# Kernel tuning notes

Measured on AMD Instinct MI355X. Metric: run time of the kernel, lower is better.

The kernel has to match this reference:

```python
import jax, jax.numpy as jnp
import numpy as np
from jax import lax

EPS = 1e-5
K = 16  # MixedOp.self.k


def conv(x, w, stride=1, pad=0, dil=1, groups=1):
    return lax.conv_general_dilated(
        x, w, (stride, stride), [(pad, pad), (pad, pad)],
        rhs_dilation=(dil, dil), feature_group_count=groups,
        dimension_numbers=('NCHW', 'OIHW', 'NCHW'))


def bn(x):
    # BatchNorm2d(affine=False) in training mode: normalize with batch stats
    m = jnp.mean(x, axis=(0, 2, 3), keepdims=True)
    v = jnp.var(x, axis=(0, 2, 3), keepdims=True)
    return (x - m) * lax.rsqrt(v + EPS)


def maxpool3(x):
    return lax.reduce_window(x, -jnp.inf, lax.max, (1, 1, 3, 3), (1, 1, 1, 1),
                             [(0, 0), (0, 0), (1, 1), (1, 1)])


def avgpool3(x):
    # AvgPool2d(3, stride=1, padding=1, count_include_pad=False)
    s = lax.reduce_window(x, 0., lax.add, (1, 1, 3, 3), (1, 1, 1, 1),
                          [(0, 0), (0, 0), (1, 1), (1, 1)])
    c = lax.reduce_window(jnp.ones_like(x), 0., lax.add, (1, 1, 3, 3),
                          (1, 1, 1, 1), [(0, 0), (0, 0), (1, 1), (1, 1)])
    return s / c


def sep_conv(x, dw1, pw1, dw2, pw2):
    C = x.shape[1]
    p = dw1.shape[-1] // 2
    h = jax.nn.relu(x)
    h = conv(h, dw1, pad=p, groups=C)
    h = bn(conv(h, pw1))
    h = jax.nn.relu(h)
    h = conv(h, dw2, pad=p, groups=C)
    return bn(conv(h, pw2))


def dil_conv(x, dw, pw):
    C = x.shape[1]
    p = (dw.shape[-1] // 2) * 2  # dilation=2 padding (3x3->2, 5x5->4)
    h = jax.nn.relu(x)
    h = conv(h, dw, pad=p, dil=2, groups=C)
    return bn(conv(h, pw))


def setup_inputs() -> dict:
    key = jax.random.key(0)
    C, B, H, W = 256, 32, 64, 64
    c_op = C // K  # 16 channels fed to each candidate op
    ks = jax.random.split(key, 17)
    g = lambda k, shp, fan: jax.random.normal(k, shp, jnp.float32) / np.sqrt(fan)
    return {
        'x': jax.random.normal(ks[0], (B, C, H, W), jnp.float32),
        # ChannelAttention se: 1x1 convs, reduction=2
        'ca_w1': g(ks[1], (C // 2, C, 1, 1), C),
        'ca_w2': g(ks[2], (C, C // 2, 1, 1), C // 2),
        # sep_conv_3x3 (two dw+pw stages)
        's3_dw1': g(ks[3], (c_op, 1, 3, 3), 9),
        's3_pw1': g(ks[4], (c_op, c_op, 1, 1), c_op),
        's3_dw2': g(ks[5], (c_op, 1, 3, 3), 9),
        's3_pw2': g(ks[6], (c_op, c_op, 1, 1), c_op),
        # sep_conv_5x5
        's5_dw1': g(ks[7], (c_op, 1, 5, 5), 25),
        's5_pw1': g(ks[8], (c_op, c_op, 1, 1), c_op),
        's5_dw2': g(ks[9], (c_op, 1, 5, 5), 25),
        's5_pw2': g(ks[10], (c_op, c_op, 1, 1), c_op),
        # dil_conv_3x3 / dil_conv_5x5
        'd3_dw': g(ks[11], (c_op, 1, 3, 3), 9),
        'd3_pw': g(ks[12], (c_op, c_op, 1, 1), c_op),
        'd5_dw': g(ks[13], (c_op, 1, 5, 5), 25),
        'd5_pw': g(ks[14], (c_op, c_op, 1, 1), c_op),
        # AttentionModule fc: channel = 8*c_op = 128, ratio = 8
        'at_w1': g(ks[15], (c_op, 8 * c_op), 8 * c_op),  # Linear(128->16)
        'at_w2': g(ks[16], (8 * c_op, c_op), c_op),      # Linear(16->128)
    }


def reference(x, ca_w1, ca_w2, s3_dw1, s3_pw1, s3_dw2, s3_pw2,
              s5_dw1, s5_pw1, s5_dw2, s5_pw2, d3_dw, d3_pw, d5_dw, d5_pw,
              at_w1, at_w2):
    B, C, H, W = x.shape
    c_sel = C // K  # number of selected channels (16)

    # ---- ChannelAttention ----
    mx = jnp.max(x, axis=(2, 3), keepdims=True)   # [B,C,1,1]
    av = jnp.mean(x, axis=(2, 3), keepdims=True)
    se = lambda z: conv(jax.nn.relu(conv(z, ca_w1)), ca_w2)
    num_list = jax.nn.sigmoid(se(mx) + se(av))    # [B,C,1,1]

    aux = x                                       # auxiliary_op = Identity (stride=1)
    xg = x * num_list

    # ---- top-k channel routing ----
    slist = jnp.sum(num_list, axis=0).reshape(C)  # sum over batch
    _, idx = lax.top_k(slist, c_sel)              # sorted, largest first
    xt = xg[:, idx]                               # gather [B,c_sel,H,W]

    # ---- 8 candidate branches (DARTS PRIMITIVES, stride=1) ----
    branches = [
        jnp.zeros_like(xt),                       # none
        bn(maxpool3(xt)),                         # max_pool_3x3 + BN
        bn(avgpool3(xt)),                         # avg_pool_3x3 + BN
        xt,                                       # skip_connect (Identity)
        sep_conv(xt, s3_dw1, s3_pw1, s3_dw2, s3_pw2),
        sep_conv(xt, s5_dw1, s5_pw1, s5_dw2, s5_pw2),
        dil_conv(xt, d3_dw, d3_pw),
        dil_conv(xt, d5_dw, d5_pw),
    ]
    temp = jnp.concatenate(branches, axis=1)      # [B, 8*c_sel, H, W]

    # ---- AttentionModule ----
    y = jnp.mean(temp, axis=(2, 3))               # [B, 8*c_sel]
    y = jax.nn.sigmoid(jax.nn.relu(y @ at_w1.T) @ at_w2.T)
    att = temp * y[:, :, None, None]
    op_attention = jnp.sum(y.reshape(B, 8, c_sel), axis=(0, 2))  # [8]

    # sum the 8 branch chunks
    out = jnp.sum(att.reshape(B, 8, c_sel, H, W), axis=1)

    # scatter back into gated x, then residual add
    xg = xg.at[:, idx].set(out)
    return xg + aux, op_attention
```

## Files before the change

kernel.cpp:

```cpp
#include <hip/hip_runtime.h>
#include <math.h>

static constexpr int B = 32, C = 256, HW = 4096, CS = 16;
static constexpr int BHW = B * HW;
static constexpr size_t IMG = (size_t)B * CS * HW;

static constexpr size_t OFF_S     = 0;
static constexpr size_t OFF_SQ    = 4096;
static constexpr size_t OFF_U     = 8192;
static constexpr size_t ACC_FLOATS= 8256;
static constexpr size_t OFF_MX    = 8256;
static constexpr size_t OFF_AV    = OFF_MX + 8192;
static constexpr size_t OFF_NUM   = OFF_AV + 8192;
static constexpr size_t OFF_Y     = OFF_NUM + 8192;
static constexpr size_t OFF_ACO   = OFF_Y + 4096;
static constexpr size_t OFF_BIAS  = OFF_ACO + 4096;
static constexpr size_t OFF_INT   = OFF_BIAS + 512;
static constexpr size_t OFF_R     = 42112;

__device__ inline float wave_sum(float v) {
  v += __shfl_down(v, 32); v += __shfl_down(v, 16); v += __shfl_down(v, 8);
  v += __shfl_down(v, 4);  v += __shfl_down(v, 2);  v += __shfl_down(v, 1);
  return v;
}
__device__ inline float wave_max(float v) {
  v = fmaxf(v, __shfl_down(v, 32)); v = fmaxf(v, __shfl_down(v, 16));
  v = fmaxf(v, __shfl_down(v, 8));  v = fmaxf(v, __shfl_down(v, 4));
  v = fmaxf(v, __shfl_down(v, 2));  v = fmaxf(v, __shfl_down(v, 1));
  return v;
}

__global__ __launch_bounds__(256) void k_stats(const float4* __restrict__ x,
                                               float* __restrict__ mx, float* __restrict__ av) {
  int bc = blockIdx.x;
  const float4* p = x + (size_t)bc * 1024;
  float mmax = -INFINITY, msum = 0.f;
  for (int i = threadIdx.x; i < 1024; i += 256) {
    float4 v = p[i];
    mmax = fmaxf(mmax, fmaxf(fmaxf(v.x, v.y), fmaxf(v.z, v.w)));
    msum += v.x + v.y + v.z + v.w;
  }
  __shared__ float rs[4], rm[4];
  float s = wave_sum(msum), m = wave_max(mmax);
  int w = threadIdx.x >> 6;
  if ((threadIdx.x & 63) == 0) { rs[w] = s; rm[w] = m; }
  __syncthreads();
  if (threadIdx.x == 0) {
    mx[bc] = fmaxf(fmaxf(rm[0], rm[1]), fmaxf(rm[2], rm[3]));
    av[bc] = (rs[0] + rs[1] + rs[2] + rs[3]) * (1.f / 4096.f);
  }
}

__global__ __launch_bounds__(128) void k_se(const float* __restrict__ mx, const float* __restrict__ av,
                                            const float* __restrict__ w1, const float* __restrict__ w2,
                                            float* __restrict__ num) {
  int b = blockIdx.x, t = threadIdx.x;
  __shared__ float zs[2][256], h[2][128];
  for (int i = t; i < 256; i += 128) { zs[0][i] = mx[b * 256 + i]; zs[1][i] = av[b * 256 + i]; }
  __syncthreads();
  {
    const float* wr = w1 + (size_t)t * 256;
    float am = 0.f, aa = 0.f;
    for (int i = 0; i < 256; i++) { float w = wr[i]; am = fmaf(w, zs[0][i], am); aa = fmaf(w, zs[1][i], aa); }
    h[0][t] = fmaxf(am, 0.f); h[1][t] = fmaxf(aa, 0.f);
  }
  __syncthreads();
  for (int c = t; c < 256; c += 128) {
    const float* wr = w2 + (size_t)c * 128;
    float sm = 0.f, sa = 0.f;
    for (int j = 0; j < 128; j++) { float w = wr[j]; sm = fmaf(w, h[0][j], sm); sa = fmaf(w, h[1][j], sa); }
    float s = sm + sa;
    num[b * 256 + c] = 1.f / (1.f + expf(-s));
  }
}

__global__ __launch_bounds__(256) void k_select(const float* __restrict__ num,
                                                int* __restrict__ idx, int* __restrict__ selmap,
                                                float* __restrict__ accbase) {
  __shared__ float s[256];
  int t = threadIdx.x;
  for (int i = t; i < (int)ACC_FLOATS; i += 256) accbase[i] = 0.f;
  float acc = 0.f;
  for (int b = 0; b < B; b++) acc += num[b * 256 + t];
  s[t] = acc; selmap[t] = -1;
  __syncthreads();
  float v = s[t];
  int rank = 0;
  for (int c = 0; c < 256; c++) {
    float o = s[c];
    rank += (o > v) || (o == v && c < t);
  }
  if (rank < 16) { idx[rank] = t; selmap[t] = rank; }
}

template<int KK, int DIL, int BN>
__device__ __forceinline__ void dw_full(const float* __restrict__ src, float sc,
                                        const float* __restrict__ w, float* __restrict__ dst,
                                        float* lt, float mu, float rs) {
  constexpr int P = (KK / 2) * DIL, TW = 64 + 2 * P;
  float wr[KK * KK];
#pragma unroll
  for (int i = 0; i < KK * KK; i++) wr[i] = w[i];
  for (int i = threadIdx.x; i < TW * TW; i += 256) {
    int ty = i / TW, tx = i - ty * TW;
    int y = ty - P, xx = tx - P;
    float v = 0.f;
    if ((unsigned)y < 64u && (unsigned)xx < 64u) {
      v = src[y * 64 + xx] * sc;
      if (BN) v = (v - mu) * rs;
      v = fmaxf(v, 0.f);
    }
    lt[i] = v;
  }
  __syncthreads();
  for (int i = threadIdx.x; i < HW; i += 256) {
    int y = i >> 6, xx = i & 63;
    const float* t0 = lt + y * TW + xx;
    float acc = 0.f;
#pragma unroll
    for (int a = 0; a < KK; a++)
#pragma unroll
      for (int q = 0; q < KK; q++)
        acc = fmaf(wr[a * KK + q], t0[a * DIL * TW + q * DIL], acc);
    dst[i] = acc;
  }
}

__device__ __forceinline__ void pools_full(const float* __restrict__ src, float sc,
                                           float* __restrict__ dmax, float* __restrict__ davg,
                                           float* __restrict__ S, float* __restrict__ SQ,
                                           int bk, float* lt, float* red) {
  for (int i = threadIdx.x; i < HW; i += 256) lt[i] = src[i] * sc;
  __syncthreads();
  float s1 = 0.f, q1 = 0.f, s2 = 0.f, q2 = 0.f, s3 = 0.f;
  for (int i = threadIdx.x; i < HW; i += 256) {
    int y = i >> 6, xx = i & 63;
    int y0 = max(y - 1, 0), y1 = min(y + 1, 63), x0 = max(xx - 1, 0), x1 = min(xx + 1, 63);
    float mx = -INFINITY, sm = 0.f;
    for (int yy = y0; yy <= y1; yy++)
      for (int cx = x0; cx <= x1; cx++) { float v = lt[yy * 64 + cx]; mx = fmaxf(mx, v); sm += v; }
    float av = sm / (float)((y1 - y0 + 1) * (x1 - x0 + 1));
    dmax[i] = mx; davg[i] = av;
    s1 += mx; q1 += mx * mx; s2 += av; q2 += av * av; s3 += lt[i];
  }
  s1 = wave_sum(s1); q1 = wave_sum(q1); s2 = wave_sum(s2); q2 = wave_sum(q2); s3 = wave_sum(s3);
  int w = threadIdx.x >> 6;
  if ((threadIdx.x & 63) == 0) { red[w] = s1; red[4 + w] = q1; red[8 + w] = s2; red[12 + w] = q2; red[16 + w] = s3; }
  __syncthreads();
  if (threadIdx.x == 0) {
    S[512 + bk]  = red[0] + red[1] + red[2] + red[3];
    SQ[512 + bk] = red[4] + red[5] + red[6] + red[7];
    S[1024 + bk] = red[8] + red[9] + red[10] + red[11];
    SQ[1024 + bk]= red[12] + red[13] + red[14] + red[15];
    S[1536 + bk] = red[16] + red[17] + red[18] + red[19];
  }
}

__global__ __launch_bounds__(256) void k_branchA(
    const float* __restrict__ x, const float* __restrict__ num, const int* __restrict__ idx,
    const float* __restrict__ d3dw, const float* __restrict__ d5dw,
    const float* __restrict__ s3dw1, const float* __restrict__ s5dw1,
    float* __restrict__ R, float* __restrict__ scr,
    float* __restrict__ S, float* __restrict__ SQ) {
  __shared__ float lt[72 * 72];
  __shared__ float red[20];
  int blk = blockIdx.x;
  int op = blk / 512, bk = blk - op * 512;
  int b = bk >> 4, k = bk & 15;
  int c = idx[k];
  float sc = num[b * 256 + c];
  const float* src = x + ((size_t)b * 256 + c) * HW;
  size_t o = (size_t)bk * HW;
  switch (op) {
    case 0: pools_full(src, sc, R + o, R + IMG + o, S, SQ, bk, lt, red); break;
    case 1: dw_full<3, 2, 0>(src, sc, d3dw + k * 9,  scr + 0 * IMG + o, lt, 0.f, 0.f); break;
    case 2: dw_full<5, 2, 0>(src, sc, d5dw + k * 25, scr + 1 * IMG + o, lt, 0.f, 0.f); break;
    case 3: dw_full<3, 1, 0>(src, sc, s3dw1 + k * 9,  scr + 2 * IMG + o, lt, 0.f, 0.f); break;
    case 4: dw_full<5, 1, 0>(src, sc, s5dw1 + k * 25, scr + 3 * IMG + o, lt, 0.f, 0.f); break;
  }
}

__device__ __forceinline__ void pw_tile(const float* __restrict__ in, const float* __restrict__ w16,
                                        float* __restrict__ out, float* __restrict__ sacc,
                                        float* __restrict__ qacc, int perB, int b, int tile,
                                        float* wsh, float* redS, float* redQ) {
  int t = threadIdx.x;
  wsh[t] = w16[t];
  size_t base = (size_t)b * 16 * HW + tile * 256;
  float sv[16];
#pragma unroll
  for (int i = 0; i < 16; i++) sv[i] = in[base + (size_t)i * HW + t];
  __syncthreads();
  int wv = t >> 6, lane = t & 63;
#pragma unroll
  for (int cc = 0; cc < 16; cc++) {
    float acc = 0.f;
#pragma unroll
    for (int i = 0; i < 16; i++) acc = fmaf(wsh[cc * 16 + i], sv[i], acc);
    out[base + (size_t)cc * HW + t] = acc;
    float s = wave_sum(acc), q = wave_sum(acc * acc);
    if (lane == 0) { redS[cc * 4 + wv] = s; redQ[cc * 4 + wv] = q; }
  }
  __syncthreads();
  if (t < 16) {
    float s = redS[t * 4] + redS[t * 4 + 1] + redS[t * 4 + 2] + redS[t * 4 + 3];
    float q = redQ[t * 4] + redQ[t * 4 + 1] + redQ[t * 4 + 2] + redQ[t * 4 + 3];
    int sl = perB ? b * 16 + t : t;
    atomicAdd(&sacc[sl], s); atomicAdd(&qacc[sl], q);
  }
}

__global__ __launch_bounds__(256) void k_branchB(
    const float* __restrict__ scr,
    const float* __restrict__ d3pw, const float* __restrict__ d5pw,
    const float* __restrict__ s3pw1, const float* __restrict__ s5pw1,
    float* __restrict__ R, float* __restrict__ t3, float* __restrict__ t5,
    float* __restrict__ S, float* __restrict__ SQ, float* __restrict__ U) {
  __shared__ float wsh[256], redS[64], redQ[64];
  int blk = blockIdx.x;
  int op = blk >> 9, rem = blk & 511;
  int b = rem >> 4, tile = rem & 15;
  switch (op) {
    case 0: pw_tile(scr + 0 * IMG, d3pw,  R + 4 * IMG, S + 6 * 512, SQ + 6 * 512, 1, b, tile, wsh, redS, redQ); break;
    case 1: pw_tile(scr + 1 * IMG, d5pw,  R + 5 * IMG, S + 7 * 512, SQ + 7 * 512, 1, b, tile, wsh, redS, redQ); break;
    case 2: pw_tile(scr + 2 * IMG, s3pw1, t3, U + 0,  U + 16, 0, b, tile, wsh, redS, redQ); break;
    case 3: pw_tile(scr + 3 * IMG, s5pw1, t5, U + 32, U + 48, 0, b, tile, wsh, redS, redQ); break;
  }
}

__global__ __launch_bounds__(256) void k_branchC(
    const float* __restrict__ t3, const float* __restrict__ t5,
    const float* __restrict__ s3dw2, const float* __restrict__ s5dw2,
    float* __restrict__ scr, const float* __restrict__ U) {
  __shared__ float lt[68 * 68];
  int blk = blockIdx.x;
  int op = blk >> 9, bk = blk & 511, k = bk & 15;
  size_t o = (size_t)bk * HW;
  if (op == 0) {
    float mu = U[k] * (1.f / (float)BHW);
    float var = U[16 + k] * (1.f / (float)BHW) - mu * mu;
    float rs = rsqrtf(var + 1e-5f);
    dw_full<3, 1, 1>(t3 + o, 1.f, s3dw2 + k * 9, scr + 0 * IMG + o, lt, mu, rs);
  } else {
    float mu = U[32 + k] * (1.f / (float)BHW);
    float var = U[48 + k] * (1.f / (float)BHW) - mu * mu;
    float rs = rsqrtf(var + 1e-5f);
    dw_full<5, 1, 1>(t5 + o, 1.f, s5dw2 + k * 25, scr + 1 * IMG + o, lt, mu, rs);
  }
}

__global__ __launch_bounds__(256) void k_branchD(
    const float* __restrict__ scr,
    const float* __restrict__ s3pw2, const float* __restrict__ s5pw2,
    float* __restrict__ R, float* __restrict__ S, float* __restrict__ SQ) {
  __shared__ float wsh[256], redS[64], redQ[64];
  int blk = blockIdx.x;
  int op = blk >> 9, rem = blk & 511;
  int b = rem >> 4, tile = rem & 15;
  if (op == 0) pw_tile(scr + 0 * IMG, s3pw2, R + 2 * IMG, S + 4 * 512, SQ + 4 * 512, 1, b, tile, wsh, redS, redQ);
  else         pw_tile(scr + 1 * IMG, s5pw2, R + 3 * IMG, S + 5 * 512, SQ + 5 * 512, 1, b, tile, wsh, redS, redQ);
}

__global__ __launch_bounds__(128) void k_att(const float* __restrict__ S, const float* __restrict__ SQ,
                                             const float* __restrict__ w1, const float* __restrict__ w2,
                                             float* __restrict__ y, float* __restrict__ aco,
                                             float* __restrict__ bia) {
  int b = blockIdx.x, t = threadIdx.x;
  __shared__ float ym[128], h[16], msh[8][16], rssh[8][16], ysh[128];
  int op = t >> 4, k = t & 15;
  bool isbn = (op == 1 || op == 2 || op >= 4);
  float m = 0.f, rsc = 0.f;
  {
    float ss = 0.f, qq = 0.f;
    for (int bb = 0; bb < B; bb++) { ss += S[op * 512 + bb * 16 + k]; qq += SQ[op * 512 + bb * 16 + k]; }
    if (isbn) {
      m = ss * (1.f / (float)BHW);
      float var = qq * (1.f / (float)BHW) - m * m;
      rsc = rsqrtf(var + 1e-5f);
    }
  }
  msh[op][k] = m; rssh[op][k] = rsc;
  float sm = S[op * 512 + b * 16 + k] * (1.f / 4096.f);
  float yme = (op == 0) ? 0.f : ((op == 3) ? sm : (sm - m) * rsc);
  ym[t] = yme;
  __syncthreads();
  if (t < 16) {
    const float* wr = w1 + (size_t)t * 128;
    float acc = 0.f;
    for (int c = 0; c < 128; c++) acc = fmaf(wr[c], ym[c], acc);
    h[t] = fmaxf(acc, 0.f);
  }
  __syncthreads();
  {
    const float* wr = w2 + (size_t)t * 16;
    float acc = 0.f;
    for (int j = 0; j < 16; j++) acc = fmaf(wr[j], h[j], acc);
    float yy = 1.f / (1.f + expf(-acc));
    ysh[t] = yy; y[b * 128 + t] = yy;
  }
  __syncthreads();
  if (t < 16) {
    float bias = 0.f;
    for (int o2 = 1; o2 < 8; o2++) {
      float yv = ysh[o2 * 16 + t];
      float a;
      if (o2 == 3) a = yv;
      else { a = yv * rssh[o2][t]; bias -= yv * rssh[o2][t] * msh[o2][t]; }
      aco[(b * 16 + t) * 8 + o2] = a;
    }
    bia[b * 16 + t] = bias;
  }
}

__global__ __launch_bounds__(256) void k_final(const float* __restrict__ x, const float* __restrict__ num,
                                               const int* __restrict__ selmap, const int* __restrict__ idx,
                                               const float* __restrict__ rbuf, const float* __restrict__ aco,
                                               const float* __restrict__ bia, const float* __restrict__ ybuf,
                                               float* __restrict__ out, float* __restrict__ out8) {
  __shared__ float sh[256];
  int bc = blockIdx.x;
  if (bc == B * C) {
    int t = threadIdx.x, op = t >> 5, lane = t & 31;
    float acc = 0.f;
    for (int i = lane; i < 512; i += 32) { int bb = i >> 4, kk = i & 15; acc += ybuf[bb * 128 + op * 16 + kk]; }
    sh[t] = acc;
    __syncthreads();
    if (lane == 0) {
      float s = 0.f;
      for (int i = 0; i < 32; i++) s += sh[op * 32 + i];
      out8[op] = s;
    }
    return;
  }
  int b = bc >> 8;
  int k = selmap[bc & 255];
  const float4* xs = (const float4*)(x + (size_t)bc * HW);
  float4* od = (float4*)(out + (size_t)bc * HW);
  if (k < 0) {
    float sc = 1.f + num[bc];
    for (int i = threadIdx.x; i < 1024; i += 256) {
      float4 v = xs[i];
      v.x *= sc; v.y *= sc; v.z *= sc; v.w *= sc;
      od[i] = v;
    }
  } else {
    int bk = b * 16 + k;
    int ci = idx[k];
    float scn = num[b * 256 + ci];
    const float4* xtp = (const float4*)(x + ((size_t)b * 256 + ci) * HW);
    const float4* r0 = (const float4*)(rbuf + ((size_t)0 * 512 + bk) * HW);
    const float4* r1 = (const float4*)(rbuf + ((size_t)1 * 512 + bk) * HW);
    const float4* r2 = (const float4*)(rbuf + ((size_t)2 * 512 + bk) * HW);
    const float4* r3 = (const float4*)(rbuf + ((size_t)3 * 512 + bk) * HW);
    const float4* r4 = (const float4*)(rbuf + ((size_t)4 * 512 + bk) * HW);
    const float4* r5 = (const float4*)(rbuf + ((size_t)5 * 512 + bk) * HW);
    float a1 = aco[bk * 8 + 1], a2 = aco[bk * 8 + 2], a3 = aco[bk * 8 + 3] * scn, a4 = aco[bk * 8 + 4];
    float a5 = aco[bk * 8 + 5], a6 = aco[bk * 8 + 6], a7 = aco[bk * 8 + 7];
    float bias = bia[bk];
    for (int i = threadIdx.x; i < 1024; i += 256) {
      float4 xv = xs[i], tv = xtp[i];
      float4 v0 = r0[i], v1 = r1[i], v2 = r2[i], v3 = r3[i], v4 = r4[i], v5 = r5[i];
      float4 o;
      o.x = xv.x + bias + a1 * v0.x + a2 * v1.x + a3 * tv.x + a4 * v2.x + a5 * v3.x + a6 * v4.x + a7 * v5.x;
      o.y = xv.y + bias + a1 * v0.y + a2 * v1.y + a3 * tv.y + a4 * v2.y + a5 * v3.y + a6 * v4.y + a7 * v5.y;
      o.z = xv.z + bias + a1 * v0.z + a2 * v1.z + a3 * tv.z + a4 * v2.z + a5 * v3.z + a6 * v4.z + a7 * v5.z;
      o.w = xv.w + bias + a1 * v0.w + a2 * v1.w + a3 * tv.w + a4 * v2.w + a5 * v3.w + a6 * v4.w + a7 * v5.w;
      od[i] = o;
    }
  }
}

extern "C" void kernel_launch(void* const* d_in, const int* in_sizes, int n_in,
                              void* d_out, int out_size, void* d_ws, size_t ws_size,
                              hipStream_t stream) {
  const float* x      = (const float*)d_in[0];
  const float* ca_w1  = (const float*)d_in[1];
  const float* ca_w2  = (const float*)d_in[2];
  const float* s3_dw1 = (const float*)d_in[3];
  const float* s3_pw1 = (const float*)d_in[4];
  const float* s3_dw2 = (const float*)d_in[5];
  const float* s3_pw2 = (const float*)d_in[6];
  const float* s5_dw1 = (const float*)d_in[7];
  const float* s5_pw1 = (const float*)d_in[8];
  const float* s5_dw2 = (const float*)d_in[9];
  const float* s5_pw2 = (const float*)d_in[10];
  const float* d3_dw  = (const float*)d_in[11];
  const float* d3_pw  = (const float*)d_in[12];
  const float* d5_dw  = (const float*)d_in[13];
  const float* d5_pw  = (const float*)d_in[14];
  const float* at_w1  = (const float*)d_in[15];
  const float* at_w2  = (const float*)d_in[16];

  float* ws = (float*)d_ws;
  float* S = ws + OFF_S;  float* SQ = ws + OFF_SQ;  float* U = ws + OFF_U;
  float* mx = ws + OFF_MX; float* av = ws + OFF_AV; float* num = ws + OFF_NUM;
  float* ybuf = ws + OFF_Y; float* aco = ws + OFF_ACO; float* bia = ws + OFF_BIAS;
  int* ib = (int*)(ws + OFF_INT);
  int* idx = ib; int* selmap = ib + 16;
  float* R = ws + OFF_R;

  float* outf = (float*)d_out;
  float* scr = outf;
  float* t3  = outf + 4 * IMG;
  float* t5  = outf + 5 * IMG;
  float* out8 = outf + (size_t)B * C * HW;

  k_stats<<<B * C, 256, 0, stream>>>((const float4*)x, mx, av);
  k_se<<<B, 128, 0, stream>>>(mx, av, ca_w1, ca_w2, num);
  k_select<<<1, 256, 0, stream>>>(num, idx, selmap, ws);
  k_branchA<<<5 * 512, 256, 0, stream>>>(x, num, idx, d3_dw, d5_dw, s3_dw1, s5_dw1, R, scr, S, SQ);
  k_branchB<<<4 * 512, 256, 0, stream>>>(scr, d3_pw, d5_pw, s3_pw1, s5_pw1, R, t3, t5, S, SQ, U);
  k_branchC<<<2 * 512, 256, 0, stream>>>(t3, t5, s3_dw2, s5_dw2, scr, U);
  k_branchD<<<2 * 512, 256, 0, stream>>>(scr, s3_pw2, s5_pw2, R, S, SQ);
  k_att<<<B, 128, 0, stream>>>(S, SQ, at_w1, at_w2, ybuf, aco, bia);
  k_final<<<B * C + 1, 256, 0, stream>>>(x, num, selmap, idx, R, aco, bia, ybuf, outf, out8);
}
```

Baseline: 213.6 us.

## Fuse middle kernels into one cooperative persistent kernel with grid syncs

Replaces the SE, select, four branch stages and attention kernels with a single cooperative persistent kernel. It loops over work units and separates stages with grid.sync(), and shared memory is reused across phases. This aims to remove launch overhead and inter-kernel gaps for small kernels. In exchange it adds grid-wide barrier cost and fixes the grid size to the occupancy-limited resident block count, which may lower latency hiding compared to oversubscribed launches.

Result: slower. 539.2 us (+152.5%).

```diff
diff --git a/kernel.cpp b/kernel.cpp
--- a/kernel.cpp
+++ b/kernel.cpp
@@ -1,5 +1,8 @@
 #include <hip/hip_runtime.h>
+#include <hip/hip_cooperative_groups.h>
 #include <math.h>
+
+namespace cg = cooperative_groups;
 
 static constexpr int B = 32, C = 256, HW = 4096, CS = 16;
 static constexpr int BHW = B * HW;
@@ -51,43 +54,42 @@
   }
 }
 
-__global__ __launch_bounds__(128) void k_se(const float* __restrict__ mx, const float* __restrict__ av,
-                                            const float* __restrict__ w1, const float* __restrict__ w2,
-                                            float* __restrict__ num) {
-  int b = blockIdx.x, t = threadIdx.x;
-  __shared__ float zs[2][256], h[2][128];
-  for (int i = t; i < 256; i += 128) { zs[0][i] = mx[b * 256 + i]; zs[1][i] = av[b * 256 + i]; }
-  __syncthreads();
-  {
+
+__device__ __forceinline__ void se_one(int b, const float* __restrict__ mx, const float* __restrict__ av,
+                                       const float* __restrict__ w1, const float* __restrict__ w2,
+                                       float* __restrict__ num, float* lt) {
+  int t = threadIdx.x;
+  __syncthreads();
+  float* zs0 = lt; float* zs1 = lt + 256; float* h0 = lt + 512; float* h1 = lt + 640;
+  zs0[t] = mx[b * 256 + t]; zs1[t] = av[b * 256 + t];
+  __syncthreads();
+  if (t < 128) {
     const float* wr = w1 + (size_t)t * 256;
     float am = 0.f, aa = 0.f;
-    for (int i = 0; i < 256; i++) { float w = wr[i]; am = fmaf(w, zs[0][i], am); aa = fmaf(w, zs[1][i], aa); }
-    h[0][t] = fmaxf(am, 0.f); h[1][t] = fmaxf(aa, 0.f);
-  }
-  __syncthreads();
-  for (int c = t; c < 256; c += 128) {
-    const float* wr = w2 + (size_t)c * 128;
+    for (int i = 0; i < 256; i++) { float w = wr[i]; am = fmaf(w, zs0[i], am); aa = fmaf(w, zs1[i], aa); }
+    h0[t] = fmaxf(am, 0.f); h1[t] = fmaxf(aa, 0.f);
+  }
+  __syncthreads();
+  {
+    const float* wr = w2 + (size_t)t * 128;
     float sm = 0.f, sa = 0.f;
-    for (int j = 0; j < 128; j++) { float w = wr[j]; sm = fmaf(w, h[0][j], sm); sa = fmaf(w, h[1][j], sa); }
-    float s = sm + sa;
-    num[b * 256 + c] = 1.f / (1.f + expf(-s));
-  }
-}
-
-__global__ __launch_bounds__(256) void k_select(const float* __restrict__ num,
-                                                int* __restrict__ idx, int* __restrict__ selmap,
-                                                float* __restrict__ accbase) {
-  __shared__ float s[256];
+    for (int j = 0; j < 128; j++) { float w = wr[j]; sm = fmaf(w, h0[j], sm); sa = fmaf(w, h1[j], sa); }
+    num[b * 256 + t] = 1.f / (1.f + expf(-(sm + sa)));
+  }
+}
+
+__device__ __forceinline__ void select_one(const float* __restrict__ num,
+                                           int* __restrict__ idx, int* __restrict__ selmap, float* lt) {
   int t = threadIdx.x;
-  for (int i = t; i < (int)ACC_FLOATS; i += 256) accbase[i] = 0.f;
+  __syncthreads();
   float acc = 0.f;
   for (int b = 0; b < B; b++) acc += num[b * 256 + t];
-  s[t] = acc; selmap[t] = -1;
-  __syncthreads();
-  float v = s[t];
+  lt[t] = acc; selmap[t] = -1;
+  __syncthreads();
+  float v = lt[t];
   int rank = 0;
   for (int c = 0; c < 256; c++) {
-    float o = s[c];
+    float o = lt[c];
     rank += (o > v) || (o == v && c < t);
   }
   if (rank < 16) { idx[rank] = t; selmap[t] = rank; }
@@ -98,6 +100,7 @@
                                         const float* __restrict__ w, float* __restrict__ dst,
                                         float* lt, float mu, float rs) {
   constexpr int P = (KK / 2) * DIL, TW = 64 + 2 * P;
+  __syncthreads();
   float wr[KK * KK];
 #pragma unroll
   for (int i = 0; i < KK * KK; i++) wr[i] = w[i];
@@ -129,7 +132,9 @@
 __device__ __forceinline__ void pools_full(const float* __restrict__ src, float sc,
                                            float* __restrict__ dmax, float* __restrict__ davg,
                                            float* __restrict__ S, float* __restrict__ SQ,
-                                           int bk, float* lt, float* red) {
+                                           int bk, float* lt) {
+  float* red = lt + 5120;
+  __syncthreads();
   for (int i = threadIdx.x; i < HW; i += 256) lt[i] = src[i] * sc;
   __syncthreads();
   float s1 = 0.f, q1 = 0.f, s2 = 0.f, q2 = 0.f, s3 = 0.f;
@@ -156,35 +161,12 @@
   }
 }
 
-__global__ __launch_bounds__(256) void k_branchA(
-    const float* __restrict__ x, const float* __restrict__ num, const int* __restrict__ idx,
-    const float* __restrict__ d3dw, const float* __restrict__ d5dw,
-    const float* __restrict__ s3dw1, const float* __restrict__ s5dw1,
-    float* __restrict__ R, float* __restrict__ scr,
-    float* __restrict__ S, float* __restrict__ SQ) {
-  __shared__ float lt[72 * 72];
-  __shared__ float red[20];
-  int blk = blockIdx.x;
-  int op = blk / 512, bk = blk - op * 512;
-  int b = bk >> 4, k = bk & 15;
-  int c = idx[k];
-  float sc = num[b * 256 + c];
-  const float* src = x + ((size_t)b * 256 + c) * HW;
-  size_t o = (size_t)bk * HW;
-  switch (op) {
-    case 0: pools_full(src, sc, R + o, R + IMG + o, S, SQ, bk, lt, red); break;
-    case 1: dw_full<3, 2, 0>(src, sc, d3dw + k * 9,  scr + 0 * IMG + o, lt, 0.f, 0.f); break;
-    case 2: dw_full<5, 2, 0>(src, sc, d5dw + k * 25, scr + 1 * IMG + o, lt, 0.f, 0.f); break;
-    case 3: dw_full<3, 1, 0>(src, sc, s3dw1 + k * 9,  scr + 2 * IMG + o, lt, 0.f, 0.f); break;
-    case 4: dw_full<5, 1, 0>(src, sc, s5dw1 + k * 25, scr + 3 * IMG + o, lt, 0.f, 0.f); break;
-  }
-}
-
 __device__ __forceinline__ void pw_tile(const float* __restrict__ in, const float* __restrict__ w16,
                                         float* __restrict__ out, float* __restrict__ sacc,
-                                        float* __restrict__ qacc, int perB, int b, int tile,
-                                        float* wsh, float* redS, float* redQ) {
+                                        float* __restrict__ qacc, int perB, int b, int tile, float* lt) {
+  float* wsh = lt; float* redS = lt + 256; float* redQ = lt + 320;
   int t = threadIdx.x;
+  __syncthreads();
   wsh[t] = w16[t];
   size_t base = (size_t)b * 16 * HW + tile * 256;
   float sv[16];
@@ -210,91 +192,39 @@
   }
 }
 
-__global__ __launch_bounds__(256) void k_branchB(
-    const float* __restrict__ scr,
-    const float* __restrict__ d3pw, const float* __restrict__ d5pw,
-    const float* __restrict__ s3pw1, const float* __restrict__ s5pw1,
-    float* __restrict__ R, float* __restrict__ t3, float* __restrict__ t5,
-    float* __restrict__ S, float* __restrict__ SQ, float* __restrict__ U) {
-  __shared__ float wsh[256], redS[64], redQ[64];
-  int blk = blockIdx.x;
-  int op = blk >> 9, rem = blk & 511;
-  int b = rem >> 4, tile = rem & 15;
-  switch (op) {
-    case 0: pw_tile(scr + 0 * IMG, d3pw,  R + 4 * IMG, S + 6 * 512, SQ + 6 * 512, 1, b, tile, wsh, redS, redQ); break;
-    case 1: pw_tile(scr + 1 * IMG, d5pw,  R + 5 * IMG, S + 7 * 512, SQ + 7 * 512, 1, b, tile, wsh, redS, redQ); break;
-    case 2: pw_tile(scr + 2 * IMG, s3pw1, t3, U + 0,  U + 16, 0, b, tile, wsh, redS, redQ); break;
-    case 3: pw_tile(scr + 3 * IMG, s5pw1, t5, U + 32, U + 48, 0, b, tile, wsh, redS, redQ); break;
-  }
-}
-
-__global__ __launch_bounds__(256) void k_branchC(
-    const float* __restrict__ t3, const float* __restrict__ t5,
-    const float* __restrict__ s3dw2, const float* __restrict__ s5dw2,
-    float* __restrict__ scr, const float* __restrict__ U) {
-  __shared__ float lt[68 * 68];
-  int blk = blockIdx.x;
-  int op = blk >> 9, bk = blk & 511, k = bk & 15;
-  size_t o = (size_t)bk * HW;
-  if (op == 0) {
-    float mu = U[k] * (1.f / (float)BHW);
-    float var = U[16 + k] * (1.f / (float)BHW) - mu * mu;
-    float rs = rsqrtf(var + 1e-5f);
-    dw_full<3, 1, 1>(t3 + o, 1.f, s3dw2 + k * 9, scr + 0 * IMG + o, lt, mu, rs);
-  } else {
-    float mu = U[32 + k] * (1.f / (float)BHW);
-    float var = U[48 + k] * (1.f / (float)BHW) - mu * mu;
-    float rs = rsqrtf(var + 1e-5f);
-    dw_full<5, 1, 1>(t5 + o, 1.f, s5dw2 + k * 25, scr + 1 * IMG + o, lt, mu, rs);
-  }
-}
-
-__global__ __launch_bounds__(256) void k_branchD(
-    const float* __restrict__ scr,
-    const float* __restrict__ s3pw2, const float* __restrict__ s5pw2,
-    float* __restrict__ R, float* __restrict__ S, float* __restrict__ SQ) {
-  __shared__ float wsh[256], redS[64], redQ[64];
-  int blk = blockIdx.x;
-  int op = blk >> 9, rem = blk & 511;
-  int b = rem >> 4, tile = rem & 15;
-  if (op == 0) pw_tile(scr + 0 * IMG, s3pw2, R + 2 * IMG, S + 4 * 512, SQ + 4 * 512, 1, b, tile, wsh, redS, redQ);
-  else         pw_tile(scr + 1 * IMG, s5pw2, R + 3 * IMG, S + 5 * 512, SQ + 5 * 512, 1, b, tile, wsh, redS, redQ);
-}
-
-__global__ __launch_bounds__(128) void k_att(const float* __restrict__ S, const float* __restrict__ SQ,
-                                             const float* __restrict__ w1, const float* __restrict__ w2,
-                                             float* __restrict__ y, float* __restrict__ aco,
-                                             float* __restrict__ bia) {
-  int b = blockIdx.x, t = threadIdx.x;
-  __shared__ float ym[128], h[16], msh[8][16], rssh[8][16], ysh[128];
-  int op = t >> 4, k = t & 15;
-  bool isbn = (op == 1 || op == 2 || op >= 4);
-  float m = 0.f, rsc = 0.f;
-  {
-    float ss = 0.f, qq = 0.f;
+__device__ __forceinline__ void att_one(int b, const float* __restrict__ S, const float* __restrict__ SQ,
+                                        const float* __restrict__ w1, const float* __restrict__ w2,
+                                        float* __restrict__ y, float* __restrict__ aco,
+                                        float* __restrict__ bia, float* lt) {
+  int t = threadIdx.x;
+  __syncthreads();
+  float* ym = lt; float* hh = lt + 128; float* msh = lt + 144; float* rssh = lt + 272; float* ysh = lt + 400;
+  if (t < 128) {
+    int op = t >> 4, k = t & 15;
+    bool isbn = (op == 1 || op == 2 || op >= 4);
+    float m = 0.f, rsc = 0.f, ss = 0.f, qq = 0.f;
     for (int bb = 0; bb < B; bb++) { ss += S[op * 512 + bb * 16 + k]; qq += SQ[op * 512 + bb * 16 + k]; }
     if (isbn) {
       m = ss * (1.f / (float)BHW);
       float var = qq * (1.f / (float)BHW) - m * m;
       rsc = rsqrtf(var + 1e-5f);
     }
-  }
-  msh[op][k] = m; rssh[op][k] = rsc;
-  float sm = S[op * 512 + b * 16 + k] * (1.f / 4096.f);
-  float yme = (op == 0) ? 0.f : ((op == 3) ? sm : (sm - m) * rsc);
-  ym[t] = yme;
+    msh[t] = m; rssh[t] = rsc;
+    float sm = S[op * 512 + b * 16 + k] * (1.f / 4096.f);
+    ym[t] = (op == 0) ? 0.f : ((op == 3) ? sm : (sm - m) * rsc);
+  }
   __syncthreads();
   if (t < 16) {
     const float* wr = w1 + (size_t)t * 128;
     float acc = 0.f;
     for (int c = 0; c < 128; c++) acc = fmaf(wr[c], ym[c], acc);
-    h[t] = fmaxf(acc, 0.f);
-  }
-  __syncthreads();
-  {
+    hh[t] = fmaxf(acc, 0.f);
+  }
+  __syncthreads();
+  if (t < 128) {
     const float* wr = w2 + (size_t)t * 16;
     float acc = 0.f;
-    for (int j = 0; j < 16; j++) acc = fmaf(wr[j], h[j], acc);
+    for (int j = 0; j < 16; j++) acc = fmaf(wr[j], hh[j], acc);
     float yy = 1.f / (1.f + expf(-acc));
     ysh[t] = yy; y[b * 128 + t] = yy;
   }
@@ -305,11 +235,100 @@
       float yv = ysh[o2 * 16 + t];
       float a;
       if (o2 == 3) a = yv;
-      else { a = yv * rssh[o2][t]; bias -= yv * rssh[o2][t] * msh[o2][t]; }
+      else { a = yv * rssh[o2 * 16 + t]; bias -= yv * rssh[o2 * 16 + t] * msh[o2 * 16 + t]; }
       aco[(b * 16 + t) * 8 + o2] = a;
     }
     bia[b * 16 + t] = bias;
   }
+}
+
+__global__ __launch_bounds__(256, 4) void k_mega(
+    const float* __restrict__ x,
+    const float* __restrict__ ca_w1, const float* __restrict__ ca_w2,
+    const float* __restrict__ s3_dw1, const float* __restrict__ s3_pw1,
+    const float* __restrict__ s3_dw2, const float* __restrict__ s3_pw2,
+    const float* __restrict__ s5_dw1, const float* __restrict__ s5_pw1,
+    const float* __restrict__ s5_dw2, const float* __restrict__ s5_pw2,
+    const float* __restrict__ d3_dw, const float* __restrict__ d3_pw,
+    const float* __restrict__ d5_dw, const float* __restrict__ d5_pw,
+    const float* __restrict__ at_w1, const float* __restrict__ at_w2,
+    float* __restrict__ ws, float* __restrict__ outf)
+{
+  cg::grid_group grid = cg::this_grid();
+  __shared__ float lt[5184];
+
+  float* S = ws + OFF_S;  float* SQ = ws + OFF_SQ;  float* U = ws + OFF_U;
+  float* mx = ws + OFF_MX; float* av = ws + OFF_AV; float* num = ws + OFF_NUM;
+  float* ybuf = ws + OFF_Y; float* aco = ws + OFF_ACO; float* bia = ws + OFF_BIAS;
+  int* ib = (int*)(ws + OFF_INT);
+  int* idx = ib; int* selmap = ib + 16;
+  float* R = ws + OFF_R;
+  float* scr = outf;
+  float* t3  = outf + 4 * IMG;
+  float* t5  = outf + 5 * IMG;
+  const int t = threadIdx.x;
+  const int nb = gridDim.x;
+
+  if (blockIdx.x < 32) se_one(blockIdx.x, mx, av, ca_w1, ca_w2, num, lt);
+  else if (blockIdx.x == 32) { for (int i = t; i < (int)ACC_FLOATS; i += 256) ws[i] = 0.f; }
+  grid.sync();
+
+  if (blockIdx.x == 0) select_one(num, idx, selmap, lt);
+  grid.sync();
+
+  for (int u = blockIdx.x; u < 5 * 512; u += nb) {
+    int op = u / 512, bk = u - op * 512;
+    int b = bk >> 4, k = bk & 15;
+    int c = idx[k];
+    float sc = num[b * 256 + c];
+    const float* src = x + ((size_t)b * 256 + c) * HW;
+    size_t o = (size_t)bk * HW;
+    switch (op) {
+      case 0: pools_full(src, sc, R + o, R + IMG + o, S, SQ, bk, lt); break;
+      case 1: dw_full<3, 2, 0>(src, sc, d3_dw + k * 9,   scr + 0 * IMG + o, lt, 0.f, 0.f); break;
+      case 2: dw_full<5, 2, 0>(src, sc, d5_dw + k * 25,  scr + 1 * IMG + o, lt, 0.f, 0.f); break;
+      case 3: dw_full<3, 1, 0>(src, sc, s3_dw1 + k * 9,  scr + 2 * IMG + o, lt, 0.f, 0.f); break;
+      case 4: dw_full<5, 1, 0>(src, sc, s5_dw1 + k * 25, scr + 3 * IMG + o, lt, 0.f, 0.f); break;
+    }
+  }
+  grid.sync();
+
+  for (int u = blockIdx.x; u < 4 * 512; u += nb) {
+    int op = u >> 9, rem = u & 511;
+    int b = rem >> 4, tile = rem & 15;
+    switch (op) {
+      case 0: pw_tile(scr + 0 * IMG, d3_pw,  R + 4 * IMG, S + 6 * 512, SQ + 6 * 512, 1, b, tile, lt); break;
+      case 1: pw_tile(scr + 1 * IMG, d5_pw,  R + 5 * IMG, S + 7 * 512, SQ + 7 * 512, 1, b, tile, lt); break;
+      case 2: pw_tile(scr + 2 * IMG, s3_pw1, t3, U + 0,  U + 16, 0, b, tile, lt); break;
+      case 3: pw_tile(scr + 3 * IMG, s5_pw1, t5, U + 32, U + 48, 0, b, tile, lt); break;
+    }
+  }
+  grid.sync();
+
+  for (int u = blockIdx.x; u < 2 * 512; u += nb) {
+    int op = u >> 9, bk = u & 511, k = bk & 15;
+    size_t o = (size_t)bk * HW;
+    if (op == 0) {
+      float mu = U[k] * (1.f / (float)BHW);
+      float var = U[16 + k] * (1.f / (float)BHW) - mu * mu;
+      dw_full<3, 1, 1>(t3 + o, 1.f, s3_dw2 + k * 9, scr + 0 * IMG + o, lt, mu, rsqrtf(var + 1e-5f));
+    } else {
+      float mu = U[32 + k] * (1.f / (float)BHW);
+      float var = U[48 + k] * (1.f / (float)BHW) - mu * mu;
+      dw_full<5, 1, 1>(t5 + o, 1.f, s5_dw2 + k * 25, scr + 1 * IMG + o, lt, mu, rsqrtf(var + 1e-5f));
+    }
+  }
+  grid.sync();
+
+  for (int u = blockIdx.x; u < 2 * 512; u += nb) {
+    int op = u >> 9, rem = u & 511;
+    int b = rem >> 4, tile = rem & 15;
+    if (op == 0) pw_tile(scr + 0 * IMG, s3_pw2, R + 2 * IMG, S + 4 * 512, SQ + 4 * 512, 1, b, tile, lt);
+    else         pw_tile(scr + 1 * IMG, s5_pw2, R + 3 * IMG, S + 5 * 512, SQ + 5 * 512, 1, b, tile, lt);
+  }
+  grid.sync();
+
+  if (blockIdx.x < 32) att_one(blockIdx.x, S, SQ, at_w1, at_w2, ybuf, aco, bia, lt);
 }
 
 __global__ __launch_bounds__(256) void k_final(const float* __restrict__ x, const float* __restrict__ num,
@@ -392,26 +411,31 @@
   const float* at_w2  = (const float*)d_in[16];
 
   float* ws = (float*)d_ws;
-  float* S = ws + OFF_S;  float* SQ = ws + OFF_SQ;  float* U = ws + OFF_U;
-  float* mx = ws + OFF_MX; float* av = ws + OFF_AV; float* num = ws + OFF_NUM;
+  float* num = ws + OFF_NUM;
   float* ybuf = ws + OFF_Y; float* aco = ws + OFF_ACO; float* bia = ws + OFF_BIAS;
   int* ib = (int*)(ws + OFF_INT);
   int* idx = ib; int* selmap = ib + 16;
   float* R = ws + OFF_R;
 
   float* outf = (float*)d_out;
-  float* scr = outf;
-  float* t3  = outf + 4 * IMG;
-  float* t5  = outf + 5 * IMG;
   float* out8 = outf + (size_t)B * C * HW;
 
-  k_stats<<<B * C, 256, 0, stream>>>((const float4*)x, mx, av);
-  k_se<<<B, 128, 0, stream>>>(mx, av, ca_w1, ca_w2, num);
-  k_select<<<1, 256, 0, stream>>>(num, idx, selmap, ws);
-  k_branchA<<<5 * 512, 256, 0, stream>>>(x, num, idx, d3_dw, d5_dw, s3_dw1, s5_dw1, R, scr, S, SQ);
-  k_branchB<<<4 * 512, 256, 0, stream>>>(scr, d3_pw, d5_pw, s3_pw1, s5_pw1, R, t3, t5, S, SQ, U);
-  k_branchC<<<2 * 512, 256, 0, stream>>>(t3, t5, s3_dw2, s5_dw2, scr, U);
-  k_branchD<<<2 * 512, 256, 0, stream>>>(scr, s3_pw2, s5_pw2, R, S, SQ);
-  k_att<<<B, 128, 0, stream>>>(S, SQ, at_w1, at_w2, ybuf, aco, bia);
+  k_stats<<<B * C, 256, 0, stream>>>((const float4*)x, ws + OFF_MX, ws + OFF_AV);
+
+  int maxb = 4;
+  (void)hipOccupancyMaxActiveBlocksPerMultiprocessor(&maxb, (const void*)k_mega, 256, 0);
+  if (maxb < 1) maxb = 1;
+  if (maxb > 8) maxb = 8;
+  int grid = maxb * 256;
+  void* args[] = {
+    (void*)&x, (void*)&ca_w1, (void*)&ca_w2,
+    (void*)&s3_dw1, (void*)&s3_pw1, (void*)&s3_dw2, (void*)&s3_pw2,
+    (void*)&s5_dw1, (void*)&s5_pw1, (void*)&s5_dw2, (void*)&s5_pw2,
+    (void*)&d3_dw, (void*)&d3_pw, (void*)&d5_dw, (void*)&d5_pw,
+    (void*)&at_w1, (void*)&at_w2,
+    (void*)&ws, (void*)&outf
+  };
+  hipLaunchCooperativeKernel((const void*)k_mega, dim3(grid), dim3(256), args, 0, stream);
+
   k_final<<<B * C + 1, 256, 0, stream>>>(x, num, selmap, idx, R, aco, bia, ybuf, outf, out8);
 }
```
